# Kernel optimization log

Hardware: AMD Instinct MI355X
Metric: run time of the kernel (lower is better)

The kernel has to match this reference:

```python
import jax, jax.numpy as jnp
import numpy as np

N = 50000
E = 800000
IN_DIM = 512
H1 = IN_DIM // 2   # 256
H2 = IN_DIM // 4   # 128
D = 8
NP_CAYLEY = D * (D - 1) // 2  # 28


def setup_inputs() -> dict:
    key = jax.random.key(0)
    ks = jax.random.split(key, 10)
    x = jax.random.normal(ks[0], (N, IN_DIM), dtype=jnp.float32)
    edge_index = jax.random.randint(ks[1], (2, E), 0, N, dtype=jnp.int64)
    s1 = 1.0 / np.sqrt(IN_DIM)
    s2 = 1.0 / np.sqrt(H1)
    s3 = 1.0 / np.sqrt(H2)
    W1l = jax.random.uniform(ks[2], (H1, IN_DIM), jnp.float32, -s1, s1)
    b1 = jax.random.uniform(ks[3], (H1,), jnp.float32, -s1, s1)
    W1r = jax.random.uniform(ks[4], (H1, IN_DIM), jnp.float32, -s1, s1)
    W2l = jax.random.uniform(ks[5], (H2, H1), jnp.float32, -s2, s2)
    b2 = jax.random.uniform(ks[6], (H2,), jnp.float32, -s2, s2)
    W2r = jax.random.uniform(ks[7], (H2, H1), jnp.float32, -s2, s2)
    Wp = jax.random.uniform(ks[8], (NP_CAYLEY, H2), jnp.float32, -s3, s3)
    bp = jax.random.uniform(ks[9], (NP_CAYLEY,), jnp.float32, -s3, s3)
    return {"x": x, "edge_index": edge_index,
            "W1l": W1l, "b1": b1, "W1r": W1r,
            "W2l": W2l, "b2": b2, "W2r": W2r,
            "Wp": Wp, "bp": bp}


def _sage_conv(x, src, dst, Wl, bl, Wr):
    # PyG SAGEConv (mean aggr): out = lin_l(mean_{j in N(i)} x_j) + lin_r(x_i)
    msg_sum = jax.ops.segment_sum(x[src], dst, num_segments=N)  # [N, F]
    deg = jax.ops.segment_sum(jnp.ones((src.shape[0],), x.dtype), dst,
                              num_segments=N)
    mean = msg_sum / jnp.maximum(deg, 1.0)[:, None]
    return mean @ Wl.T + bl + x @ Wr.T


def _cayley(params):
    # params: [N, d(d-1)/2] -> skew A, then O = (I - A)^{-1} (I + A)
    iu, ju = jnp.triu_indices(D, k=1)  # row-major i<j matches torch loop order
    n = params.shape[0]
    A = jnp.zeros((n, D, D), params.dtype)
    A = A.at[:, iu, ju].set(params)
    A = A.at[:, ju, iu].set(-params)
    I = jnp.eye(D, dtype=params.dtype)
    return jnp.linalg.solve(I[None] - A, I[None] + A)


def reference(x, edge_index, W1l, b1, W1r, W2l, b2, W2r, Wp, bp):
    src, dst = edge_index[0], edge_index[1]
    h = jax.nn.relu(_sage_conv(x, src, dst, W1l, b1, W1r))
    h = jax.nn.relu(_sage_conv(h, src, dst, W2l, b2, W2r))
    params = h @ Wp.T + bp  # [N, 28]
    return _cayley(params)  # [N, 8, 8]
```

## Files before the change

kernel.cpp:

```cpp
#include <hip/hip_runtime.h>
#include <hip/hip_bf16.h>


#define WS_ALIGN(x) (((x) + 255) & ~size_t(255))

typedef __attribute__((ext_vector_type(8))) short short8;
typedef __attribute__((ext_vector_type(4))) float floatx4;

static __device__ __forceinline__ ushort f2b(float f) {
    unsigned u = __builtin_bit_cast(unsigned, f);
    u = (u + 0x7fffu + ((u >> 16) & 1u)) >> 16;
    return (ushort)u;
}
static __device__ __forceinline__ float b2f(ushort h) {
    unsigned u = ((unsigned)h) << 16;
    return __builtin_bit_cast(float, u);
}


__global__ void hist_kernel(const int* __restrict__ dst, int* __restrict__ deg, int E) {
    int e = blockIdx.x * blockDim.x + threadIdx.x;
    if (e < E) atomicAdd(&deg[dst[e]], 1);
}

__global__ __launch_bounds__(256)
void scan_phase1(const int* __restrict__ deg, int* __restrict__ bsum, int n) {
    __shared__ int red[256];
    const int t = threadIdx.x;
    const int i = blockIdx.x * 1024 + t * 4;
    int s = 0;
    if (i + 4 <= n) {
        int4 v = *reinterpret_cast<const int4*>(&deg[i]);
        s = v.x + v.y + v.z + v.w;
    } else {
        for (int k = i; k < n; ++k) s += deg[k];
    }
    red[t] = s;
    __syncthreads();
#pragma unroll
    for (int off = 128; off > 0; off >>= 1) {
        if (t < off) red[t] += red[t + off];
        __syncthreads();
    }
    if (t == 0) bsum[blockIdx.x] = red[0];
}

__global__ __launch_bounds__(256)
void scan_phase2(int* __restrict__ bsum, int* __restrict__ rowptr, int nb, int n) {
    __shared__ int sh[256];
    const int t = threadIdx.x;
    int orig = (t < nb) ? bsum[t] : 0;
    sh[t] = orig;
    __syncthreads();
#pragma unroll
    for (int off = 1; off < 256; off <<= 1) {
        int v = (t >= off) ? sh[t - off] : 0;
        __syncthreads();
        sh[t] += v;
        __syncthreads();
    }
    if (t < nb) bsum[t] = sh[t] - orig;
    if (t == 255) rowptr[n] = sh[255];
}

__global__ __launch_bounds__(256)
void scan_phase3(const int* __restrict__ deg, const int* __restrict__ bsum,
                 int* __restrict__ rowptr, int n) {
    __shared__ int red[256];
    const int t = threadIdx.x;
    const int i = blockIdx.x * 1024 + t * 4;
    int v0 = 0, v1 = 0, v2 = 0, v3 = 0;
    if (i + 4 <= n) {
        int4 v = *reinterpret_cast<const int4*>(&deg[i]);
        v0 = v.x; v1 = v.y; v2 = v.z; v3 = v.w;
    } else {
        if (i     < n) v0 = deg[i];
        if (i + 1 < n) v1 = deg[i + 1];
        if (i + 2 < n) v2 = deg[i + 2];
        if (i + 3 < n) v3 = deg[i + 3];
    }
    int s = v0 + v1 + v2 + v3;
    red[t] = s;
    __syncthreads();
#pragma unroll
    for (int off = 1; off < 256; off <<= 1) {
        int u = (t >= off) ? red[t - off] : 0;
        __syncthreads();
        red[t] += u;
        __syncthreads();
    }
    int pre = bsum[blockIdx.x] + red[t] - s;
    if (i + 4 <= n) {
        int4 o;
        o.x = pre; o.y = pre + v0; o.z = pre + v0 + v1; o.w = pre + v0 + v1 + v2;
        *reinterpret_cast<int4*>(&rowptr[i]) = o;
    } else {
        if (i     < n) rowptr[i]     = pre;
        if (i + 1 < n) rowptr[i + 1] = pre + v0;
        if (i + 2 < n) rowptr[i + 2] = pre + v0 + v1;
        if (i + 3 < n) rowptr[i + 3] = pre + v0 + v1 + v2;
    }
}

__global__ void scatter_kernel(const int* __restrict__ src, const int* __restrict__ dst,
                               const int* __restrict__ rowptr, int* __restrict__ cursor,
                               int* __restrict__ adj, int E) {
    int e = blockIdx.x * blockDim.x + threadIdx.x;
    if (e < E) {
        int d = dst[e];
        int p = atomicAdd(&cursor[d], 1);
        adj[rowptr[d] + p] = src[e];
    }
}


__global__ void cast_kernel(const float* __restrict__ src, ushort* __restrict__ dst, int n8) {
    for (int i = blockIdx.x * blockDim.x + threadIdx.x; i < n8; i += gridDim.x * blockDim.x) {
        const float4* s4 = reinterpret_cast<const float4*>(src + (size_t)i * 8);
        float4 v0 = s4[0], v1 = s4[1];
        short8 o;
        o[0] = (short)f2b(v0.x); o[1] = (short)f2b(v0.y);
        o[2] = (short)f2b(v0.z); o[3] = (short)f2b(v0.w);
        o[4] = (short)f2b(v1.x); o[5] = (short)f2b(v1.y);
        o[6] = (short)f2b(v1.z); o[7] = (short)f2b(v1.w);
        *reinterpret_cast<short8*>(dst + (size_t)i * 8) = o;
    }
}

__global__ void build_wcat(const float* __restrict__ W1l, const float* __restrict__ W1r,
                           const float* __restrict__ W2l, const float* __restrict__ W2r,
                           ushort* __restrict__ Wc1, ushort* __restrict__ Wc2) {
    int idx = blockIdx.x * blockDim.x + threadIdx.x;
    const int n1 = (512 * 512) / 8;
    const int n2 = (256 * 256) / 8;
    const float* src;
    ushort* dst;
    if (idx < n1) {
        int e = idx * 8;
        int row = e >> 9, col = e & 511;
        src = (row < 256) ? &W1l[row * 512 + col] : &W1r[(row - 256) * 512 + col];
        dst = &Wc1[e];
    } else if (idx < n1 + n2) {
        int e = (idx - n1) * 8;
        int row = e >> 8, col = e & 255;
        src = (row < 128) ? &W2l[row * 256 + col] : &W2r[(row - 128) * 256 + col];
        dst = &Wc2[e];
    } else {
        return;
    }
    const float4* s4 = reinterpret_cast<const float4*>(src);
    float4 v0 = s4[0], v1 = s4[1];
    short8 o;
    o[0] = (short)f2b(v0.x); o[1] = (short)f2b(v0.y);
    o[2] = (short)f2b(v0.z); o[3] = (short)f2b(v0.w);
    o[4] = (short)f2b(v1.x); o[5] = (short)f2b(v1.y);
    o[6] = (short)f2b(v1.z); o[7] = (short)f2b(v1.w);
    *reinterpret_cast<short8*>(dst) = o;
}


__global__ __launch_bounds__(256)
void gemm_bf16(const ushort* __restrict__ A, const ushort* __restrict__ B,
               ushort* __restrict__ Cl, ushort* __restrict__ Cr,
               int M, int K, int S, int gx) {
    __shared__ ushort As[128 * 64];
    __shared__ ushort Bs[128 * 64];
    const int tid  = threadIdx.x;
    const int wave = tid >> 6;
    const int lane = tid & 63;

    const int W = gridDim.x;
    const int q = W >> 3, r = W & 7;
    const int xcd = blockIdx.x & 7, slot = blockIdx.x >> 3;
    const int w = (xcd < r ? xcd * (q + 1) : r * (q + 1) + (xcd - r) * q) + slot;
    const int row0 = (w / gx) * 128;
    const int col0 = (w % gx) * 128;

    const int wm = (wave & 1) * 64;
    const int wn = (wave >> 1) * 64;

    floatx4 acc[4][4];
#pragma unroll
    for (int i = 0; i < 4; ++i)
#pragma unroll
        for (int j = 0; j < 4; ++j)
            acc[i][j] = (floatx4){0.f, 0.f, 0.f, 0.f};

    const int rsub = lane >> 3;
    const int ksw  = ((lane & 7) * 16) ^ (rsub << 4);

    for (int k0 = 0; k0 < K; k0 += 64) {
#pragma unroll
        for (int i = 0; i < 4; ++i) {
            int chunk = wave * 4 + i;
            int rr = chunk * 8 + rsub;
            int grow = row0 + rr;
            if (grow >= M) grow = M - 1;
            const char* srcp = (const char*)(A + (size_t)grow * K + k0) + ksw;
            __builtin_amdgcn_global_load_lds(
                (const __attribute__((address_space(1))) unsigned int*)srcp,
                (__attribute__((address_space(3))) unsigned int*)(&As[chunk * 512]),
                16, 0, 0);
        }
#pragma unroll
        for (int i = 0; i < 4; ++i) {
            int chunk = wave * 4 + i;
            int rr = chunk * 8 + rsub;
            int gcol = col0 + rr;
            const char* srcp = (const char*)(B + (size_t)gcol * K + k0) + ksw;
            __builtin_amdgcn_global_load_lds(
                (const __attribute__((address_space(1))) unsigned int*)srcp,
                (__attribute__((address_space(3))) unsigned int*)(&Bs[chunk * 512]),
                16, 0, 0);
        }
        __syncthreads();

#pragma unroll
        for (int kk = 0; kk < 2; ++kk) {
            short8 af[4], bf[4];
            const int kb = (kk * 64 + ((lane >> 4) << 4)) ^ ((lane & 7) << 4);
#pragma unroll
            for (int im = 0; im < 4; ++im) {
                int rr = wm + im * 16 + (lane & 15);
                af[im] = *reinterpret_cast<const short8*>((const char*)As + rr * 128 + kb);
            }
#pragma unroll
            for (int in = 0; in < 4; ++in) {
                int rr = wn + in * 16 + (lane & 15);
                bf[in] = *reinterpret_cast<const short8*>((const char*)Bs + rr * 128 + kb);
            }
#pragma unroll
            for (int im = 0; im < 4; ++im)
#pragma unroll
                for (int in = 0; in < 4; ++in)
                    acc[im][in] = __builtin_amdgcn_mfma_f32_16x16x32_bf16(
                        af[im], bf[in], acc[im][in], 0, 0, 0);
        }
        __syncthreads();
    }

    ushort* Cbase = (col0 < S) ? Cl : Cr;
    const int cb = (col0 < S) ? col0 : col0 - S;
#pragma unroll
    for (int im = 0; im < 4; ++im) {
#pragma unroll
        for (int reg = 0; reg < 4; ++reg) {
            int rr = row0 + wm + im * 16 + ((lane >> 4) << 2) + reg;
            if (rr < M) {
                size_t base = (size_t)rr * S + cb + wn + (lane & 15);
#pragma unroll
                for (int in = 0; in < 4; ++in)
                    Cbase[base + in * 16] = f2b(acc[im][in][reg]);
            }
        }
    }
}


template <int LPN>
__global__ __launch_bounds__(256)
void aggregate_bf16(const ushort* __restrict__ Yl, const ushort* __restrict__ Yr,
                    const float* __restrict__ bias,
                    const int* __restrict__ rowptr, const int* __restrict__ adj,
                    ushort* __restrict__ H, int n) {
    constexpr int F = LPN * 8;
    const int grp = threadIdx.x / LPN;
    const int sub = threadIdx.x % LPN;
    const int node = blockIdx.x * (256 / LPN) + grp;
    if (node >= n) return;
    const int c = sub * 8;
    const int start = rowptr[node], end = rowptr[node + 1];

    float acc[8];
#pragma unroll
    for (int v = 0; v < 8; ++v) acc[v] = 0.f;

    int e = start;
    for (; e + 8 <= end; e += 8) {
        short8 rr[8];
#pragma unroll
        for (int u = 0; u < 8; ++u) {
            int s = adj[e + u];
            rr[u] = *reinterpret_cast<const short8*>(&Yl[(size_t)s * F + c]);
        }
#pragma unroll
        for (int v = 0; v < 8; ++v) {
            float t0 = (b2f((ushort)rr[0][v]) + b2f((ushort)rr[1][v])) +
                       (b2f((ushort)rr[2][v]) + b2f((ushort)rr[3][v]));
            float t1 = (b2f((ushort)rr[4][v]) + b2f((ushort)rr[5][v])) +
                       (b2f((ushort)rr[6][v]) + b2f((ushort)rr[7][v]));
            acc[v] += t0 + t1;
        }
    }
    for (; e + 4 <= end; e += 4) {
        int s0 = adj[e + 0], s1 = adj[e + 1], s2 = adj[e + 2], s3 = adj[e + 3];
        short8 r0 = *reinterpret_cast<const short8*>(&Yl[(size_t)s0 * F + c]);
        short8 r1 = *reinterpret_cast<const short8*>(&Yl[(size_t)s1 * F + c]);
        short8 r2 = *reinterpret_cast<const short8*>(&Yl[(size_t)s2 * F + c]);
        short8 r3 = *reinterpret_cast<const short8*>(&Yl[(size_t)s3 * F + c]);
#pragma unroll
        for (int v = 0; v < 8; ++v)
            acc[v] += (b2f((ushort)r0[v]) + b2f((ushort)r1[v])) +
                      (b2f((ushort)r2[v]) + b2f((ushort)r3[v]));
    }
    for (; e < end; ++e) {
        int s = adj[e];
        short8 rr = *reinterpret_cast<const short8*>(&Yl[(size_t)s * F + c]);
#pragma unroll
        for (int v = 0; v < 8; ++v) acc[v] += b2f((ushort)rr[v]);
    }

    const int d = end - start;
    const float inv = 1.0f / (float)(d > 0 ? d : 1);
    short8 sv = *reinterpret_cast<const short8*>(&Yr[(size_t)node * F + c]);
    float4 bv0 = *reinterpret_cast<const float4*>(&bias[c]);
    float4 bv1 = *reinterpret_cast<const float4*>(&bias[c + 4]);
    float bb[8] = {bv0.x, bv0.y, bv0.z, bv0.w, bv1.x, bv1.y, bv1.z, bv1.w};
    short8 o;
#pragma unroll
    for (int v = 0; v < 8; ++v)
        o[v] = (short)f2b(fmaxf(acc[v] * inv + b2f((ushort)sv[v]) + bb[v], 0.f));
    *reinterpret_cast<short8*>(&H[(size_t)node * F + c]) = o;
}


__global__ __launch_bounds__(256)
void params_kernel(const ushort* __restrict__ H2, const float* __restrict__ Wp,
                   const float* __restrict__ bp, float* __restrict__ P, int n) {
    __shared__ float WpS[32 * 132];
    __shared__ float bpS[32];
    for (int t = threadIdx.x; t < 32 * 132; t += 256) WpS[t] = 0.f;
    if (threadIdx.x < 32) bpS[threadIdx.x] = (threadIdx.x < 28) ? bp[threadIdx.x] : 0.f;
    __syncthreads();
    for (int t = threadIdx.x; t < 28 * 128; t += 256) {
        int r = t >> 7, c = t & 127;
        WpS[r * 132 + c] = Wp[t];
    }
    __syncthreads();

    const int node = blockIdx.x * 32 + (threadIdx.x >> 3);
    const int l = threadIdx.x & 7;
    if (node >= n) return;

    short8 h8[16];
    const short8* hp = reinterpret_cast<const short8*>(&H2[(size_t)node * 128]);
#pragma unroll
    for (int q = 0; q < 16; ++q) h8[q] = hp[q];

    float acc0 = bpS[l], acc1 = bpS[l + 8], acc2 = bpS[l + 16], acc3 = bpS[l + 24];
#pragma unroll
    for (int q = 0; q < 32; ++q) {
        float h0 = b2f((ushort)h8[q >> 1][(q & 1) * 4 + 0]);
        float h1 = b2f((ushort)h8[q >> 1][(q & 1) * 4 + 1]);
        float h2 = b2f((ushort)h8[q >> 1][(q & 1) * 4 + 2]);
        float h3 = b2f((ushort)h8[q >> 1][(q & 1) * 4 + 3]);
        float4 w0 = *reinterpret_cast<const float4*>(&WpS[(l +  0) * 132 + 4 * q]);
        float4 w1 = *reinterpret_cast<const float4*>(&WpS[(l +  8) * 132 + 4 * q]);
        float4 w2 = *reinterpret_cast<const float4*>(&WpS[(l + 16) * 132 + 4 * q]);
        float4 w3 = *reinterpret_cast<const float4*>(&WpS[(l + 24) * 132 + 4 * q]);
        acc0 += h0 * w0.x + h1 * w0.y + h2 * w0.z + h3 * w0.w;
        acc1 += h0 * w1.x + h1 * w1.y + h2 * w1.z + h3 * w1.w;
        acc2 += h0 * w2.x + h1 * w2.y + h2 * w2.z + h3 * w2.w;
        acc3 += h0 * w3.x + h1 * w3.y + h2 * w3.z + h3 * w3.w;
    }
    float* pout = &P[(size_t)node * 32];
    pout[l]      = acc0;
    pout[l + 8]  = acc1;
    pout[l + 16] = acc2;
    pout[l + 24] = acc3;
}


__global__ __launch_bounds__(256)
void cayley_kernel(const float* __restrict__ P, float* __restrict__ Out, int n) {
    int i = blockIdx.x * blockDim.x + threadIdx.x;
    if (i >= n) return;
    float p[28];
    const float4* pp = reinterpret_cast<const float4*>(&P[(size_t)i * 32]);
#pragma unroll
    for (int q = 0; q < 7; ++q) {
        float4 v = pp[q];
        p[4 * q + 0] = v.x; p[4 * q + 1] = v.y;
        p[4 * q + 2] = v.z; p[4 * q + 3] = v.w;
    }

    float M_[8][8], B_[8][8];
#pragma unroll
    for (int r = 0; r < 8; ++r)
#pragma unroll
        for (int c = 0; c < 8; ++c) {
            M_[r][c] = (r == c) ? 1.f : 0.f;
            B_[r][c] = (r == c) ? 1.f : 0.f;
        }
    {
        int idx = 0;
#pragma unroll
        for (int r = 0; r < 8; ++r)
#pragma unroll
            for (int c = r + 1; c < 8; ++c) {
                float a = p[idx++];
                M_[r][c] -= a;  M_[c][r] += a;
                B_[r][c] += a;  B_[c][r] -= a;
            }
    }
#pragma unroll
    for (int col = 0; col < 8; ++col) {
        float inv = 1.0f / M_[col][col];
#pragma unroll
        for (int c = 0; c < 8; ++c) { M_[col][c] *= inv; B_[col][c] *= inv; }
#pragma unroll
        for (int r = 0; r < 8; ++r) {
            if (r == col) continue;
            float f = M_[r][col];
#pragma unroll
            for (int c = 0; c < 8; ++c) {
                M_[r][c] -= f * M_[col][c];
                B_[r][c] -= f * B_[col][c];
            }
        }
    }
    float* out = &Out[(size_t)i * 64];
#pragma unroll
    for (int r = 0; r < 8; ++r) {
        float4 o0 = make_float4(B_[r][0], B_[r][1], B_[r][2], B_[r][3]);
        float4 o1 = make_float4(B_[r][4], B_[r][5], B_[r][6], B_[r][7]);
        *reinterpret_cast<float4*>(&out[r * 8 + 0]) = o0;
        *reinterpret_cast<float4*>(&out[r * 8 + 4]) = o1;
    }
}


extern "C" void kernel_launch(void* const* d_in, const int* in_sizes, int n_in,
                              void* d_out, int out_size, void* d_ws, size_t ws_size,
                              hipStream_t stream) {
    const float* x   = (const float*)d_in[0];
    const int*   ei  = (const int*)d_in[1];
    const float* W1l = (const float*)d_in[2];
    const float* b1  = (const float*)d_in[3];
    const float* W1r = (const float*)d_in[4];
    const float* W2l = (const float*)d_in[5];
    const float* b2  = (const float*)d_in[6];
    const float* W2r = (const float*)d_in[7];
    const float* Wp  = (const float*)d_in[8];
    const float* bp  = (const float*)d_in[9];
    float* out = (float*)d_out;

    const int IN_DIM = 512;
    const int N = in_sizes[0] / IN_DIM;
    const int E = in_sizes[1] / 2;

    char* ws = (char*)d_ws;
    size_t off = 0;
    int* deg      = (int*)(ws + off); off = WS_ALIGN(off + (size_t)N * 4);
    int* rowptr   = (int*)(ws + off); off = WS_ALIGN(off + (size_t)(N + 1) * 4);
    int* cursor   = (int*)(ws + off); off = WS_ALIGN(off + (size_t)N * 4);
    int* bsum     = (int*)(ws + off); off = WS_ALIGN(off + (size_t)256 * 4);
    int* adj      = (int*)(ws + off); off = WS_ALIGN(off + (size_t)E * 4);
    ushort* xb    = (ushort*)(ws + off); off = WS_ALIGN(off + (size_t)N * 512 * 2);
    ushort* Yl    = (ushort*)(ws + off); off = WS_ALIGN(off + (size_t)N * 256 * 2);
    ushort* Yr    = (ushort*)(ws + off); off = WS_ALIGN(off + (size_t)N * 256 * 2);
    ushort* h1    = (ushort*)(ws + off); off = WS_ALIGN(off + (size_t)N * 256 * 2);
    ushort* zl    = (ushort*)(ws + off); off = WS_ALIGN(off + (size_t)N * 128 * 2);
    ushort* zr    = (ushort*)(ws + off); off = WS_ALIGN(off + (size_t)N * 128 * 2);
    ushort* Wc1   = (ushort*)(ws + off); off = WS_ALIGN(off + (size_t)512 * 512 * 2);
    ushort* Wc2   = (ushort*)(ws + off); off = WS_ALIGN(off + (size_t)256 * 256 * 2);
    float*  Pp    = (float*)(ws + off);  off = WS_ALIGN(off + (size_t)N * 32 * 4);

    const int* src = ei;
    const int* dst = ei + E;

    hipMemsetAsync(deg, 0, (size_t)N * 4, stream);
    hipMemsetAsync(cursor, 0, (size_t)N * 4, stream);

    int eb = (E + 255) / 256;
    int nb = (N + 1023) / 1024;
    hist_kernel<<<eb, 256, 0, stream>>>(dst, deg, E);
    scan_phase1<<<nb, 256, 0, stream>>>(deg, bsum, N);
    scan_phase2<<<1, 256, 0, stream>>>(bsum, rowptr, nb, N);
    scan_phase3<<<nb, 256, 0, stream>>>(deg, bsum, rowptr, N);
    scatter_kernel<<<eb, 256, 0, stream>>>(src, dst, rowptr, cursor, adj, E);

    cast_kernel<<<2048, 256, 0, stream>>>(x, xb, N * 512 / 8);
    build_wcat<<<((512 * 512 + 256 * 256) / 8 + 255) / 256, 256, 0, stream>>>(
        W1l, W1r, W2l, W2r, Wc1, Wc2);

    int gm = (N + 127) / 128;

    gemm_bf16<<<gm * 4, 256, 0, stream>>>(xb, Wc1, Yl, Yr, N, 512, 256, 4);
    aggregate_bf16<32><<<(N + 7) / 8, 256, 0, stream>>>(Yl, Yr, b1, rowptr, adj, h1, N);

    gemm_bf16<<<gm * 2, 256, 0, stream>>>(h1, Wc2, zl, zr, N, 256, 128, 2);
    ushort* h2 = Yl;
    aggregate_bf16<16><<<(N + 15) / 16, 256, 0, stream>>>(zl, zr, b2, rowptr, adj, h2, N);

    params_kernel<<<(N + 31) / 32, 256, 0, stream>>>(h2, Wp, bp, Pp, N);
    cayley_kernel<<<(N + 255) / 256, 256, 0, stream>>>(Pp, out, N);
}
```

Before: 298.2 us.

## Slice neighbor aggregation by feature columns and merge prep kernels

The aggregation kernels now use a 2D grid where each block handles 32 nodes for one 32-column feature slice, with 8 lanes per node each loading 4 bf16 values. The aim is to shrink each gather's working set so it stays in cache across blocks in the same slice. Separately, the x cast, degree histogram and weight packing are fused into one launch to cut launch overhead. In exchange, each block reads rowptr and adj once per slice, and each gather moves 8 bytes instead of 16.

```diff
diff --git a/kernel.cpp b/kernel.cpp
--- a/kernel.cpp
+++ b/kernel.cpp
@@ -18,10 +18,58 @@
 }
 
 
-__global__ void hist_kernel(const int* __restrict__ dst, int* __restrict__ deg, int E) {
-    int e = blockIdx.x * blockDim.x + threadIdx.x;
-    if (e < E) atomicAdd(&deg[dst[e]], 1);
-}
+__global__ __launch_bounds__(256)
+void prep_kernel(const float* __restrict__ x, ushort* __restrict__ xb, int n8, int cb,
+                 const int* __restrict__ dst, int* __restrict__ deg, int E, int eb,
+                 const float* __restrict__ W1l, const float* __restrict__ W1r,
+                 const float* __restrict__ W2l, const float* __restrict__ W2r,
+                 ushort* __restrict__ Wc1, ushort* __restrict__ Wc2) {
+    const int b = blockIdx.x;
+    const int tid = threadIdx.x;
+    if (b < cb) {
+        for (int i = b * 256 + tid; i < n8; i += cb * 256) {
+            const float4* s4 = reinterpret_cast<const float4*>(x + (size_t)i * 8);
+            float4 v0 = s4[0], v1 = s4[1];
+            short8 o;
+            o[0] = (short)f2b(v0.x); o[1] = (short)f2b(v0.y);
+            o[2] = (short)f2b(v0.z); o[3] = (short)f2b(v0.w);
+            o[4] = (short)f2b(v1.x); o[5] = (short)f2b(v1.y);
+            o[6] = (short)f2b(v1.z); o[7] = (short)f2b(v1.w);
+            *reinterpret_cast<short8*>(xb + (size_t)i * 8) = o;
+        }
+    } else if (b < cb + eb) {
+        int e = (b - cb) * 256 + tid;
+        if (e < E) atomicAdd(&deg[dst[e]], 1);
+    } else {
+        int idx = (b - cb - eb) * 256 + tid;
+        const int n1 = (512 * 512) / 8;
+        const int n2 = (256 * 256) / 8;
+        const float* src;
+        ushort* dstp;
+        if (idx < n1) {
+            int e = idx * 8;
+            int row = e >> 9, col = e & 511;
+            src = (row < 256) ? &W1l[row * 512 + col] : &W1r[(row - 256) * 512 + col];
+            dstp = &Wc1[e];
+        } else if (idx < n1 + n2) {
+            int e = (idx - n1) * 8;
+            int row = e >> 8, col = e & 255;
+            src = (row < 128) ? &W2l[row * 256 + col] : &W2r[(row - 128) * 256 + col];
+            dstp = &Wc2[e];
+        } else {
+            return;
+        }
+        const float4* s4 = reinterpret_cast<const float4*>(src);
+        float4 v0 = s4[0], v1 = s4[1];
+        short8 o;
+        o[0] = (short)f2b(v0.x); o[1] = (short)f2b(v0.y);
+        o[2] = (short)f2b(v0.z); o[3] = (short)f2b(v0.w);
+        o[4] = (short)f2b(v1.x); o[5] = (short)f2b(v1.y);
+        o[6] = (short)f2b(v1.z); o[7] = (short)f2b(v1.w);
+        *reinterpret_cast<short8*>(dstp) = o;
+    }
+}
+
 
 __global__ __launch_bounds__(256)
 void scan_phase1(const int* __restrict__ deg, int* __restrict__ bsum, int n) {
@@ -114,51 +162,6 @@
 }
 
 
-__global__ void cast_kernel(const float* __restrict__ src, ushort* __restrict__ dst, int n8) {
-    for (int i = blockIdx.x * blockDim.x + threadIdx.x; i < n8; i += gridDim.x * blockDim.x) {
-        const float4* s4 = reinterpret_cast<const float4*>(src + (size_t)i * 8);
-        float4 v0 = s4[0], v1 = s4[1];
-        short8 o;
-        o[0] = (short)f2b(v0.x); o[1] = (short)f2b(v0.y);
-        o[2] = (short)f2b(v0.z); o[3] = (short)f2b(v0.w);
-        o[4] = (short)f2b(v1.x); o[5] = (short)f2b(v1.y);
-        o[6] = (short)f2b(v1.z); o[7] = (short)f2b(v1.w);
-        *reinterpret_cast<short8*>(dst + (size_t)i * 8) = o;
-    }
-}
-
-__global__ void build_wcat(const float* __restrict__ W1l, const float* __restrict__ W1r,
-                           const float* __restrict__ W2l, const float* __restrict__ W2r,
-                           ushort* __restrict__ Wc1, ushort* __restrict__ Wc2) {
-    int idx = blockIdx.x * blockDim.x + threadIdx.x;
-    const int n1 = (512 * 512) / 8;
-    const int n2 = (256 * 256) / 8;
-    const float* src;
-    ushort* dst;
-    if (idx < n1) {
-        int e = idx * 8;
-        int row = e >> 9, col = e & 511;
-        src = (row < 256) ? &W1l[row * 512 + col] : &W1r[(row - 256) * 512 + col];
-        dst = &Wc1[e];
-    } else if (idx < n1 + n2) {
-        int e = (idx - n1) * 8;
-        int row = e >> 8, col = e & 255;
-        src = (row < 128) ? &W2l[row * 256 + col] : &W2r[(row - 128) * 256 + col];
-        dst = &Wc2[e];
-    } else {
-        return;
-    }
-    const float4* s4 = reinterpret_cast<const float4*>(src);
-    float4 v0 = s4[0], v1 = s4[1];
-    short8 o;
-    o[0] = (short)f2b(v0.x); o[1] = (short)f2b(v0.y);
-    o[2] = (short)f2b(v0.z); o[3] = (short)f2b(v0.w);
-    o[4] = (short)f2b(v1.x); o[5] = (short)f2b(v1.y);
-    o[6] = (short)f2b(v1.z); o[7] = (short)f2b(v1.w);
-    *reinterpret_cast<short8*>(dst) = o;
-}
-
-
 __global__ __launch_bounds__(256)
 void gemm_bf16(const ushort* __restrict__ A, const ushort* __restrict__ B,
                ushort* __restrict__ Cl, ushort* __restrict__ Cr,
@@ -257,70 +260,50 @@
 }
 
 
-template <int LPN>
-__global__ __launch_bounds__(256)
-void aggregate_bf16(const ushort* __restrict__ Yl, const ushort* __restrict__ Yr,
-                    const float* __restrict__ bias,
-                    const int* __restrict__ rowptr, const int* __restrict__ adj,
-                    ushort* __restrict__ H, int n) {
-    constexpr int F = LPN * 8;
-    const int grp = threadIdx.x / LPN;
-    const int sub = threadIdx.x % LPN;
-    const int node = blockIdx.x * (256 / LPN) + grp;
+template <int F>
+__global__ __launch_bounds__(256)
+void agg_sliced(const ushort* __restrict__ Yl, const ushort* __restrict__ Yr,
+                const float* __restrict__ bias,
+                const int* __restrict__ rowptr, const int* __restrict__ adj,
+                ushort* __restrict__ H, int n) {
+    const int g   = threadIdx.x >> 3;
+    const int sub = threadIdx.x & 7;
+    const int node = blockIdx.x * 32 + g;
     if (node >= n) return;
-    const int c = sub * 8;
+    const int c = blockIdx.y * 32 + sub * 4;
     const int start = rowptr[node], end = rowptr[node + 1];
 
-    float acc[8];
-#pragma unroll
-    for (int v = 0; v < 8; ++v) acc[v] = 0.f;
-
+    float a0 = 0.f, a1 = 0.f, a2 = 0.f, a3 = 0.f;
     int e = start;
     for (; e + 8 <= end; e += 8) {
-        short8 rr[8];
+        ushort4 rr[8];
 #pragma unroll
         for (int u = 0; u < 8; ++u) {
             int s = adj[e + u];
-            rr[u] = *reinterpret_cast<const short8*>(&Yl[(size_t)s * F + c]);
-        }
-#pragma unroll
-        for (int v = 0; v < 8; ++v) {
-            float t0 = (b2f((ushort)rr[0][v]) + b2f((ushort)rr[1][v])) +
-                       (b2f((ushort)rr[2][v]) + b2f((ushort)rr[3][v]));
-            float t1 = (b2f((ushort)rr[4][v]) + b2f((ushort)rr[5][v])) +
-                       (b2f((ushort)rr[6][v]) + b2f((ushort)rr[7][v]));
-            acc[v] += t0 + t1;
-        }
-    }
-    for (; e + 4 <= end; e += 4) {
-        int s0 = adj[e + 0], s1 = adj[e + 1], s2 = adj[e + 2], s3 = adj[e + 3];
-        short8 r0 = *reinterpret_cast<const short8*>(&Yl[(size_t)s0 * F + c]);
-        short8 r1 = *reinterpret_cast<const short8*>(&Yl[(size_t)s1 * F + c]);
-        short8 r2 = *reinterpret_cast<const short8*>(&Yl[(size_t)s2 * F + c]);
-        short8 r3 = *reinterpret_cast<const short8*>(&Yl[(size_t)s3 * F + c]);
-#pragma unroll
-        for (int v = 0; v < 8; ++v)
-            acc[v] += (b2f((ushort)r0[v]) + b2f((ushort)r1[v])) +
-                      (b2f((ushort)r2[v]) + b2f((ushort)r3[v]));
+            rr[u] = *reinterpret_cast<const ushort4*>(&Yl[(size_t)s * F + c]);
+        }
+#pragma unroll
+        for (int u = 0; u < 8; ++u) {
+            a0 += b2f(rr[u].x); a1 += b2f(rr[u].y);
+            a2 += b2f(rr[u].z); a3 += b2f(rr[u].w);
+        }
     }
     for (; e < end; ++e) {
         int s = adj[e];
-        short8 rr = *reinterpret_cast<const short8*>(&Yl[(size_t)s * F + c]);
-#pragma unroll
-        for (int v = 0; v < 8; ++v) acc[v] += b2f((ushort)rr[v]);
+        ushort4 rr = *reinterpret_cast<const ushort4*>(&Yl[(size_t)s * F + c]);
+        a0 += b2f(rr.x); a1 += b2f(rr.y); a2 += b2f(rr.z); a3 += b2f(rr.w);
     }
 
     const int d = end - start;
     const float inv = 1.0f / (float)(d > 0 ? d : 1);
-    short8 sv = *reinterpret_cast<const short8*>(&Yr[(size_t)node * F + c]);
-    float4 bv0 = *reinterpret_cast<const float4*>(&bias[c]);
-    float4 bv1 = *reinterpret_cast<const float4*>(&bias[c + 4]);
-    float bb[8] = {bv0.x, bv0.y, bv0.z, bv0.w, bv1.x, bv1.y, bv1.z, bv1.w};
-    short8 o;
-#pragma unroll
-    for (int v = 0; v < 8; ++v)
-        o[v] = (short)f2b(fmaxf(acc[v] * inv + b2f((ushort)sv[v]) + bb[v], 0.f));
-    *reinterpret_cast<short8*>(&H[(size_t)node * F + c]) = o;
+    ushort4 sv = *reinterpret_cast<const ushort4*>(&Yr[(size_t)node * F + c]);
+    float4 bv = *reinterpret_cast<const float4*>(&bias[c]);
+    ushort4 o;
+    o.x = f2b(fmaxf(a0 * inv + b2f(sv.x) + bv.x, 0.f));
+    o.y = f2b(fmaxf(a1 * inv + b2f(sv.y) + bv.y, 0.f));
+    o.z = f2b(fmaxf(a2 * inv + b2f(sv.z) + bv.z, 0.f));
+    o.w = f2b(fmaxf(a3 * inv + b2f(sv.w) + bv.w, 0.f));
+    *reinterpret_cast<ushort4*>(&H[(size_t)node * F + c]) = o;
 }
 
 
@@ -472,26 +455,28 @@
     hipMemsetAsync(deg, 0, (size_t)N * 4, stream);
     hipMemsetAsync(cursor, 0, (size_t)N * 4, stream);
 
-    int eb = (E + 255) / 256;
-    int nb = (N + 1023) / 1024;
-    hist_kernel<<<eb, 256, 0, stream>>>(dst, deg, E);
+    const int eb = (E + 255) / 256;
+    const int cb = 1024;
+    const int wb = ((512 * 512 + 256 * 256) / 8 + 255) / 256;
+    const int nb = (N + 1023) / 1024;
+
+    prep_kernel<<<cb + eb + wb, 256, 0, stream>>>(
+        x, xb, N * 512 / 8, cb, dst, deg, E, eb,
+        W1l, W1r, W2l, W2r, Wc1, Wc2);
     scan_phase1<<<nb, 256, 0, stream>>>(deg, bsum, N);
     scan_phase2<<<1, 256, 0, stream>>>(bsum, rowptr, nb, N);
     scan_phase3<<<nb, 256, 0, stream>>>(deg, bsum, rowptr, N);
     scatter_kernel<<<eb, 256, 0, stream>>>(src, dst, rowptr, cursor, adj, E);
 
-    cast_kernel<<<2048, 256, 0, stream>>>(x, xb, N * 512 / 8);
-    build_wcat<<<((512 * 512 + 256 * 256) / 8 + 255) / 256, 256, 0, stream>>>(
-        W1l, W1r, W2l, W2r, Wc1, Wc2);
-
     int gm = (N + 127) / 128;
+    int ab = (N + 31) / 32;
 
     gemm_bf16<<<gm * 4, 256, 0, stream>>>(xb, Wc1, Yl, Yr, N, 512, 256, 4);
-    aggregate_bf16<32><<<(N + 7) / 8, 256, 0, stream>>>(Yl, Yr, b1, rowptr, adj, h1, N);
+    agg_sliced<256><<<dim3(ab, 8), 256, 0, stream>>>(Yl, Yr, b1, rowptr, adj, h1, N);
 
     gemm_bf16<<<gm * 2, 256, 0, stream>>>(h1, Wc2, zl, zr, N, 256, 128, 2);
     ushort* h2 = Yl;
-    aggregate_bf16<16><<<(N + 15) / 16, 256, 0, stream>>>(zl, zr, b2, rowptr, adj, h2, N);
+    agg_sliced<128><<<dim3(ab, 4), 256, 0, stream>>>(zl, zr, b2, rowptr, adj, h2, N);
 
     params_kernel<<<(N + 31) / 32, 256, 0, stream>>>(h2, Wp, bp, Pp, N);
     cayley_kernel<<<(N + 255) / 256, 256, 0, stream>>>(Pp, out, N);
```

Result: slower. 319.5 us (+7.1%).
